# Kernel optimization log

Measured on AMD Instinct MI355X. Metric: run time of the kernel, lower is better.

The kernel has to match this reference:

```python
import jax, jax.numpy as jnp
import numpy as np

B_, S_, F_ = 4096, 512, 3
MAT_PTS = 128
N_OUT = 3
N_LAT = MAT_PTS * N_OUT  # 384
E, NU = 3130.0, 0.3
A_H, B_H, C_H = 64.8, 33.6, 0.003407
MU = E / (2.0 * (1.0 + NU))
LAM = E * NU / ((1.0 + NU) * (1.0 - 2.0 * NU))
NEWTON_ITERS = 12
VEC1 = jnp.array([1.0, 1.0, 1.0, 0.0], dtype=jnp.float32)  # identity in Voigt-4 (xx,yy,zz,xy)


def setup_inputs() -> dict:
    key = jax.random.key(0)
    k1, k2, k3 = jax.random.split(key, 3)
    x = jax.random.normal(k1, (B_, S_, F_), dtype=jnp.float32) * 0.01
    W1 = jax.random.normal(k2, (N_LAT, F_), dtype=jnp.float32) * (1.0 / np.sqrt(F_))
    W2 = jax.random.normal(k3, (N_OUT, N_LAT), dtype=jnp.float32) * (1.0 / np.sqrt(N_LAT))
    return {"x": x, "W1": W1, "W2": W2}


def _j2_update(state, eps):
    """J2 plane-strain return mapping with exponential hardening.
    state: (ep [N,4] tensorial plastic strain, kappa [N] eq. plastic strain)
    eps:   [N,3] engineering strain (exx, eyy, gxy).
    Returns new state and stress [N,3] (sxx, syy, sxy)."""
    ep, kappa = state
    e = jnp.stack([eps[:, 0], eps[:, 1], jnp.zeros_like(eps[:, 0]), 0.5 * eps[:, 2]], axis=-1)
    ee = e - ep                                   # elastic strain, tensorial
    tr = ee[:, 0] + ee[:, 1] + ee[:, 2]
    sig = 2.0 * MU * ee + LAM * tr[:, None] * VEC1  # trial stress (xx,yy,zz,xy)
    p = (sig[:, 0] + sig[:, 1] + sig[:, 2]) / 3.0
    s = sig - p[:, None] * VEC1                    # deviatoric
    q = jnp.sqrt(1.5 * (s[:, 0] ** 2 + s[:, 1] ** 2 + s[:, 2] ** 2 + 2.0 * s[:, 3] ** 2))
    sy = A_H - B_H * jnp.exp(-kappa / C_H)
    f = q - sy                                     # yield function (trial)

    def newton_step(dg, _):
        kp = kappa + dg
        r = q - 3.0 * MU * dg - (A_H - B_H * jnp.exp(-kp / C_H))
        dr = -3.0 * MU - (B_H / C_H) * jnp.exp(-kp / C_H)
        dg_new = jnp.maximum(dg - r / dr, 0.0)
        return dg_new, None

    dg0 = jnp.zeros_like(q)
    dg, _ = jax.lax.scan(newton_step, dg0, None, length=NEWTON_ITERS)
    dg = jnp.where(f > 0.0, dg, 0.0)
    q_safe = jnp.maximum(q, 1e-12)
    n = 1.5 * s / q_safe[:, None]                  # flow direction
    sig_new = sig - 2.0 * MU * dg[:, None] * n
    ep_new = ep + dg[:, None] * n
    kappa_new = kappa + dg
    stress = jnp.stack([sig_new[:, 0], sig_new[:, 1], sig_new[:, 3]], axis=-1)
    return (ep_new, kappa_new), stress


def _forward(x, W1, W2):
    B, S, F = x.shape
    N = B * MAT_PTS  # material points across the batch
    # fc1 is time-independent: apply to all timesteps at once
    h = jnp.einsum('bsf,lf->bsl', x, W1)                 # [B,S,n_latents]
    eps_seq = h.reshape(B, S, MAT_PTS, F_).transpose(1, 0, 2, 3).reshape(S, N, F_)
    ep0 = jnp.zeros((N, 4), dtype=x.dtype)
    k0 = jnp.zeros((N,), dtype=x.dtype)
    _, stresses = jax.lax.scan(_j2_update, (ep0, k0), eps_seq)  # [S,N,3]
    lat = stresses.reshape(S, B, N_LAT).transpose(1, 0, 2)      # [B,S,n_latents]
    return jnp.einsum('bsl,ol->bso', lat, W2)                   # [B,S,n_outputs]


def reference(x, W1, W2):
    return _forward(x, W1, W2)
```

## Files before the change

kernel.cpp:

```cpp
#include <hip/hip_runtime.h>
#include <math.h>

#define S_LEN 512
#define CH 8
#define NSEG 128
#define TBL_L0 -22.0f
#define TBL_INVH 4.0f
#define TBL_H 0.25f

typedef float v2f __attribute__((ext_vector_type(2)));

__device__ __forceinline__ float fast_rcp(float x) { return __builtin_amdgcn_rcpf(x); }
__device__ __forceinline__ float fast_rsq(float x) { return __builtin_amdgcn_rsqf(x); }
__device__ __forceinline__ float exp2s(float x)    { return __builtin_amdgcn_exp2f(x); }
__device__ __forceinline__ v2f rsqv(v2f a)  { return (v2f){fast_rsq(a.x), fast_rsq(a.y)}; }
__device__ __forceinline__ v2f maxv(v2f a, v2f b) { return __builtin_elementwise_max(a, b); }

template <int CTRL>
__device__ __forceinline__ float dpp_add(float v) {
    int vi = __builtin_bit_cast(int, v);
    int t  = __builtin_amdgcn_update_dpp(vi, vi, CTRL, 0xF, 0xF, true);
    return v + __builtin_bit_cast(float, t);
}

__global__ __launch_bounds__(128, 4) void prnn_kernel(
    const float* __restrict__ x,
    const float* __restrict__ W1,
    const float* __restrict__ W2,
    float* __restrict__ out)
{
    const double MUd = 3130.0 / 2.6;
    const double Cd  = 0.003407;
    const double K2d = 1.4426950408889634 / Cd;
    const float MU      = (float)MUd;
    const float THREE_MU= (float)(3.0 * MUd);
    const float C43     = (float)(4.0 * MUd / 3.0);
    const float C23     = (float)(2.0 * MUd / 3.0);
    const float CP      = (float)(7825.0 / 3.0);
    const float Cf      = (float)Cd;
    const float R3M     = (float)(1.0 / (3.0 * MUd));
    const float AR3M    = (float)(64.8 / (3.0 * MUd));
    const float MQ      = (float)(-K2d / (3.0 * MUd));
    const float KA0     = (float)(1.4492898 + (64.8 / (3.0 * MUd)) * K2d);
    const float K2      = (float)K2d;
    const float LOG2E   = 1.4426950408889634f;
    const float LN08    = (float)(0.8 * 0.6931471805599453);

    const int tid  = threadIdx.x;
    const int lane = tid & 63;
    const int wv   = tid >> 6;
    const int b    = blockIdx.x * 2 + wv;

    __shared__ float2 xs01[2][S_LEN];
    __shared__ float  xs2g[2][S_LEN];
    __shared__ float  part[2][CH][3][17];
    __shared__ float2 wtab[NSEG];

    {
        float wn = 0.0f;
        if (tid <= NSEG) {
            const float s = TBL_L0 + (float)tid * TBL_H;
            const float z = exp2s(s);
            float w = fmaxf(LN08 * s, z * (1.0f - z));
            #pragma unroll
            for (int it = 0; it < 4; ++it) {
                const float y   = exp2s(w * LOG2E);
                const float g   = w * y;
                const float F   = g - z;
                const float Fp  = g + y;
                const float den = Fp*Fp - 0.5f*((F*y)*(2.0f + w));
                w = w - (F*Fp)*fast_rcp(den);
            }
            wn = w;
            ((float*)wtab)[tid] = wn;
        }
        __syncthreads();
        float wnext = 0.0f;
        if (tid < NSEG) wnext = ((float*)wtab)[tid + 1];
        __syncthreads();
        if (tid < NSEG) {
            const float sl = (wnext - wn) * (Cf * TBL_INVH);
            const float bi = Cf * wn - sl * (TBL_L0 + (float)tid * TBL_H);
            wtab[tid] = (float2){sl, bi};
        }
        __syncthreads();
    }

    v2f D0[3], D1[3], D3[3], pv[3];
    #pragma unroll
    for (int f = 0; f < 3; ++f) {
        const int mA = lane, mB = lane + 64;
        v2f av = (v2f){ W1[(mA*3 + 0)*3 + f], W1[(mB*3 + 0)*3 + f] };
        v2f bv = (v2f){ W1[(mA*3 + 1)*3 + f], W1[(mB*3 + 1)*3 + f] };
        v2f cv = (v2f){ W1[(mA*3 + 2)*3 + f], W1[(mB*3 + 2)*3 + f] };
        D0[f] = C43*av - C23*bv;
        D1[f] = C43*bv - C23*av;
        D3[f] = MU*cv;
        pv[f] = CP*(av + bv);
    }
    v2f w2[3][3];
    #pragma unroll
    for (int o = 0; o < 3; ++o)
        #pragma unroll
        for (int j = 0; j < 3; ++j)
            w2[o][j] = (v2f){ W2[o*384 + lane*3 + j], W2[o*384 + (lane+64)*3 + j] };

    float gsel0, gsel1, gsel2;
    {
        v2f w2s[3];
        #pragma unroll
        for (int o = 0; o < 3; ++o) w2s[o] = w2[o][0] + w2[o][1];
        float G[3][3];
        #pragma unroll
        for (int o = 0; o < 3; ++o)
            #pragma unroll
            for (int f = 0; f < 3; ++f) {
                v2f gv = w2s[o] * pv[f];
                float g = gv.x + gv.y;
                #pragma unroll
                for (int m = 1; m < 64; m <<= 1) g += __shfl_xor(g, m, 64);
                G[o][f] = g;
            }
        const int ro = lane % 3;
        gsel0 = (ro == 0) ? G[0][0] : (ro == 1) ? G[1][0] : G[2][0];
        gsel1 = (ro == 0) ? G[0][1] : (ro == 1) ? G[1][1] : G[2][1];
        gsel2 = (ro == 0) ? G[0][2] : (ro == 1) ? G[1][2] : G[2][2];
    }

    const float* xb = x + (size_t)b * (S_LEN*3);
    for (int i = lane; i < S_LEN; i += 64) {
        xs01[wv][i] = (float2){ xb[i*3 + 0], xb[i*3 + 1] };
        xs2g[wv][i] = xb[i*3 + 2];
    }

    v2f sd0 = (v2f){0.f,0.f}, sd1 = sd0, sd3 = sd0;
    v2f ka2 = (v2f){KA0, KA0};
    float xp0 = 0.f, xp1 = 0.f, xp2 = 0.f;
    float* outb = out + (size_t)b * (S_LEN*3);

    #pragma unroll 1
    for (int tc = 0; tc < S_LEN; tc += CH) {
        #pragma unroll
        for (int tt = 0; tt < CH; ++tt) {
            const int t = tc + tt;
            const float2 x01 = xs01[wv][t];
            const float  xv2 = xs2g[wv][t];
            const float dx0 = x01.x - xp0, dx1 = x01.y - xp1, dx2 = xv2 - xp2;
            xp0 = x01.x; xp1 = x01.y; xp2 = xv2;

            v2f d0 = D0[0]*dx0 + D0[1]*dx1 + D0[2]*dx2 + sd0;
            v2f d1 = D1[0]*dx0 + D1[1]*dx1 + D1[2]*dx2 + sd1;
            v2f d3 = D3[0]*dx0 + D3[1]*dx1 + D3[2]*dx2 + sd3;

            v2f h   = d0*d0 + d1*d1 + d0*d1 + d3*d3;
            v2f dot = maxv(3.0f*h, (v2f){1e-24f,1e-24f});
            v2f qi  = rsqv(dot);
            v2f q   = dot * qi;

            v2f u0  = q*R3M - AR3M;
            v2f l2z = q*MQ + ka2;

            const float fix = __builtin_fmaf(l2z.x, TBL_INVH, -TBL_L0*TBL_INVH);
            const float fiy = __builtin_fmaf(l2z.y, TBL_INVH, -TBL_L0*TBL_INVH);
            int ix = (int)fix; ix = ix < 0 ? 0 : (ix > NSEG-1 ? NSEG-1 : ix);
            int iy = (int)fiy; iy = iy < 0 ? 0 : (iy > NSEG-1 ? NSEG-1 : iy);
            const float2 tx = wtab[ix];
            const float2 ty = wtab[iy];
            v2f cw = (v2f){ __builtin_fmaf(tx.x, l2z.x, tx.y),
                            __builtin_fmaf(ty.x, l2z.y, ty.y) };
            v2f dg = maxv(u0 + cw, (v2f){0.f,0.f});

            v2f n3q = -THREE_MU*qi;
            v2f u   = dg*n3q + 1.0f;
            sd0 = u*d0; sd1 = u*d1; sd3 = u*d3;
            ka2 = ka2 - K2*dg;

            v2f a0 = w2[0][0]*sd0 + w2[0][1]*sd1 + w2[0][2]*sd3;
            v2f a1 = w2[1][0]*sd0 + w2[1][1]*sd1 + w2[1][2]*sd3;
            v2f a2 = w2[2][0]*sd0 + w2[2][1]*sd1 + w2[2][2]*sd3;
            float c0 = a0.x + a0.y;
            float c1 = a1.x + a1.y;
            float c2 = a2.x + a2.y;

            c0 = dpp_add<0xB1>(c0); c0 = dpp_add<0x4E>(c0);
            c1 = dpp_add<0xB1>(c1); c1 = dpp_add<0x4E>(c1);
            c2 = dpp_add<0xB1>(c2); c2 = dpp_add<0x4E>(c2);
            if ((lane & 3) == 0) {
                const int g16 = lane >> 2;
                part[wv][tt][0][g16] = c0;
                part[wv][tt][1][g16] = c1;
                part[wv][tt][2][g16] = c2;
            }
        }
        if (lane < 24) {
            const int rtt = lane / 3;
            float s = 0.0f;
            #pragma unroll
            for (int g16 = 0; g16 < 16; ++g16) s += part[wv][rtt][lane - rtt*3][g16];
            const float2 xf01 = xs01[wv][tc + rtt];
            const float  xf2  = xs2g[wv][tc + rtt];
            s = __builtin_fmaf(gsel0, xf01.x, s);
            s = __builtin_fmaf(gsel1, xf01.y, s);
            s = __builtin_fmaf(gsel2, xf2,    s);
            outb[tc*3 + lane] = s;
        }
    }
}

extern "C" void kernel_launch(void* const* d_in, const int* in_sizes, int n_in,
                              void* d_out, int out_size, void* d_ws, size_t ws_size,
                              hipStream_t stream) {
    const float* x  = (const float*)d_in[0];
    const float* W1 = (const float*)d_in[1];
    const float* W2 = (const float*)d_in[2];
    float* out = (float*)d_out;
    prnn_kernel<<<2048, 128, 0, stream>>>(x, W1, W2, out);
}
```

Measured before the change: 307.0 us.

## Read x via wave-uniform scalar loads instead of LDS staging, drop v2f packing

Removes the LDS staging of each sequence's x and instead makes the batch index wave-uniform with readfirstlane, so x values can be fetched with scalar loads directly from global memory. The packed v2f arithmetic is replaced by scalar per-point FMA chains, and the table index upper clamp is dropped. This is meant to cut LDS traffic and instruction count in the serial time loop. In exchange, each step now does global and scalar-cache loads on the critical path, and dropping the clamp risks out-of-range table reads.

```diff
diff --git a/kernel.cpp b/kernel.cpp
--- a/kernel.cpp
+++ b/kernel.cpp
@@ -8,13 +8,9 @@
 #define TBL_INVH 4.0f
 #define TBL_H 0.25f
 
-typedef float v2f __attribute__((ext_vector_type(2)));
-
 __device__ __forceinline__ float fast_rcp(float x) { return __builtin_amdgcn_rcpf(x); }
 __device__ __forceinline__ float fast_rsq(float x) { return __builtin_amdgcn_rsqf(x); }
 __device__ __forceinline__ float exp2s(float x)    { return __builtin_amdgcn_exp2f(x); }
-__device__ __forceinline__ v2f rsqv(v2f a)  { return (v2f){fast_rsq(a.x), fast_rsq(a.y)}; }
-__device__ __forceinline__ v2f maxv(v2f a, v2f b) { return __builtin_elementwise_max(a, b); }
 
 template <int CTRL>
 __device__ __forceinline__ float dpp_add(float v) {
@@ -49,10 +45,8 @@
     const int tid  = threadIdx.x;
     const int lane = tid & 63;
     const int wv   = tid >> 6;
-    const int b    = blockIdx.x * 2 + wv;
-
-    __shared__ float2 xs01[2][S_LEN];
-    __shared__ float  xs2g[2][S_LEN];
+    const int bs   = __builtin_amdgcn_readfirstlane(blockIdx.x * 2 + wv);
+
     __shared__ float  part[2][CH][3][17];
     __shared__ float2 wtab[NSEG];
 
@@ -86,37 +80,38 @@
         __syncthreads();
     }
 
-    v2f D0[3], D1[3], D3[3], pv[3];
+    float D0[2][3], D1[2][3], D3[2][3], pvv[2][3], w2[2][3][3];
     #pragma unroll
-    for (int f = 0; f < 3; ++f) {
-        const int mA = lane, mB = lane + 64;
-        v2f av = (v2f){ W1[(mA*3 + 0)*3 + f], W1[(mB*3 + 0)*3 + f] };
-        v2f bv = (v2f){ W1[(mA*3 + 1)*3 + f], W1[(mB*3 + 1)*3 + f] };
-        v2f cv = (v2f){ W1[(mA*3 + 2)*3 + f], W1[(mB*3 + 2)*3 + f] };
-        D0[f] = C43*av - C23*bv;
-        D1[f] = C43*bv - C23*av;
-        D3[f] = MU*cv;
-        pv[f] = CP*(av + bv);
-    }
-    v2f w2[3][3];
-    #pragma unroll
-    for (int o = 0; o < 3; ++o)
-        #pragma unroll
-        for (int j = 0; j < 3; ++j)
-            w2[o][j] = (v2f){ W2[o*384 + lane*3 + j], W2[o*384 + (lane+64)*3 + j] };
+    for (int p = 0; p < 2; ++p) {
+        const int m = lane + 64*p;
+        #pragma unroll
+        for (int f = 0; f < 3; ++f) {
+            const float av = W1[(m*3 + 0)*3 + f];
+            const float bv = W1[(m*3 + 1)*3 + f];
+            const float cv = W1[(m*3 + 2)*3 + f];
+            D0[p][f]  = C43*av - C23*bv;
+            D1[p][f]  = C43*bv - C23*av;
+            D3[p][f]  = MU*cv;
+            pvv[p][f] = CP*(av + bv);
+        }
+        #pragma unroll
+        for (int o = 0; o < 3; ++o)
+            #pragma unroll
+            for (int j = 0; j < 3; ++j)
+                w2[p][o][j] = W2[o*384 + m*3 + j];
+    }
 
     float gsel0, gsel1, gsel2;
     {
-        v2f w2s[3];
-        #pragma unroll
-        for (int o = 0; o < 3; ++o) w2s[o] = w2[o][0] + w2[o][1];
         float G[3][3];
         #pragma unroll
         for (int o = 0; o < 3; ++o)
             #pragma unroll
             for (int f = 0; f < 3; ++f) {
-                v2f gv = w2s[o] * pv[f];
-                float g = gv.x + gv.y;
+                float g = 0.0f;
+                #pragma unroll
+                for (int p = 0; p < 2; ++p)
+                    g += (w2[p][o][0] + w2[p][o][1]) * pvv[p][f];
                 #pragma unroll
                 for (int m = 1; m < 64; m <<= 1) g += __shfl_xor(g, m, 64);
                 G[o][f] = g;
@@ -127,60 +122,71 @@
         gsel2 = (ro == 0) ? G[0][2] : (ro == 1) ? G[1][2] : G[2][2];
     }
 
-    const float* xb = x + (size_t)b * (S_LEN*3);
-    for (int i = lane; i < S_LEN; i += 64) {
-        xs01[wv][i] = (float2){ xb[i*3 + 0], xb[i*3 + 1] };
-        xs2g[wv][i] = xb[i*3 + 2];
-    }
-
-    v2f sd0 = (v2f){0.f,0.f}, sd1 = sd0, sd3 = sd0;
-    v2f ka2 = (v2f){KA0, KA0};
+    const float* xbs  = x   + (size_t)bs * (S_LEN*3);
+    float*       outb = out + (size_t)bs * (S_LEN*3);
+
+    float sd0[2] = {0.f,0.f}, sd1[2] = {0.f,0.f}, sd3[2] = {0.f,0.f};
+    float ka2[2] = {KA0, KA0};
     float xp0 = 0.f, xp1 = 0.f, xp2 = 0.f;
-    float* outb = out + (size_t)b * (S_LEN*3);
+
+    const int rtt0 = (lane < 24) ? (lane / 3) : 0;
 
     #pragma unroll 1
     for (int tc = 0; tc < S_LEN; tc += CH) {
+        const float* xrow = xbs + (tc + rtt0)*3;
+        const float fx0 = xrow[0], fx1 = xrow[1], fx2 = xrow[2];
+
         #pragma unroll
         for (int tt = 0; tt < CH; ++tt) {
             const int t = tc + tt;
-            const float2 x01 = xs01[wv][t];
-            const float  xv2 = xs2g[wv][t];
-            const float dx0 = x01.x - xp0, dx1 = x01.y - xp1, dx2 = xv2 - xp2;
-            xp0 = x01.x; xp1 = x01.y; xp2 = xv2;
-
-            v2f d0 = D0[0]*dx0 + D0[1]*dx1 + D0[2]*dx2 + sd0;
-            v2f d1 = D1[0]*dx0 + D1[1]*dx1 + D1[2]*dx2 + sd1;
-            v2f d3 = D3[0]*dx0 + D3[1]*dx1 + D3[2]*dx2 + sd3;
-
-            v2f h   = d0*d0 + d1*d1 + d0*d1 + d3*d3;
-            v2f dot = maxv(3.0f*h, (v2f){1e-24f,1e-24f});
-            v2f qi  = rsqv(dot);
-            v2f q   = dot * qi;
-
-            v2f u0  = q*R3M - AR3M;
-            v2f l2z = q*MQ + ka2;
-
-            const float fix = __builtin_fmaf(l2z.x, TBL_INVH, -TBL_L0*TBL_INVH);
-            const float fiy = __builtin_fmaf(l2z.y, TBL_INVH, -TBL_L0*TBL_INVH);
-            int ix = (int)fix; ix = ix < 0 ? 0 : (ix > NSEG-1 ? NSEG-1 : ix);
-            int iy = (int)fiy; iy = iy < 0 ? 0 : (iy > NSEG-1 ? NSEG-1 : iy);
-            const float2 tx = wtab[ix];
-            const float2 ty = wtab[iy];
-            v2f cw = (v2f){ __builtin_fmaf(tx.x, l2z.x, tx.y),
-                            __builtin_fmaf(ty.x, l2z.y, ty.y) };
-            v2f dg = maxv(u0 + cw, (v2f){0.f,0.f});
-
-            v2f n3q = -THREE_MU*qi;
-            v2f u   = dg*n3q + 1.0f;
-            sd0 = u*d0; sd1 = u*d1; sd3 = u*d3;
-            ka2 = ka2 - K2*dg;
-
-            v2f a0 = w2[0][0]*sd0 + w2[0][1]*sd1 + w2[0][2]*sd3;
-            v2f a1 = w2[1][0]*sd0 + w2[1][1]*sd1 + w2[1][2]*sd3;
-            v2f a2 = w2[2][0]*sd0 + w2[2][1]*sd1 + w2[2][2]*sd3;
-            float c0 = a0.x + a0.y;
-            float c1 = a1.x + a1.y;
-            float c2 = a2.x + a2.y;
+            const float x0 = xbs[t*3 + 0];
+            const float x1 = xbs[t*3 + 1];
+            const float x2 = xbs[t*3 + 2];
+            const float dx0 = x0 - xp0, dx1 = x1 - xp1, dx2 = x2 - xp2;
+            xp0 = x0; xp1 = x1; xp2 = x2;
+
+            float cc[2][3];
+            #pragma unroll
+            for (int p = 0; p < 2; ++p) {
+                const float d0 = __builtin_fmaf(D0[p][0], dx0,
+                                  __builtin_fmaf(D0[p][1], dx1,
+                                  __builtin_fmaf(D0[p][2], dx2, sd0[p])));
+                const float d1 = __builtin_fmaf(D1[p][0], dx0,
+                                  __builtin_fmaf(D1[p][1], dx1,
+                                  __builtin_fmaf(D1[p][2], dx2, sd1[p])));
+                const float d3 = __builtin_fmaf(D3[p][0], dx0,
+                                  __builtin_fmaf(D3[p][1], dx1,
+                                  __builtin_fmaf(D3[p][2], dx2, sd3[p])));
+
+                const float h   = __builtin_fmaf(d0, d0,
+                                   __builtin_fmaf(d1, d1,
+                                   __builtin_fmaf(d0, d1, d3*d3)));
+                const float dot = fmaxf(3.0f*h, 1e-24f);
+                const float qi  = fast_rsq(dot);
+                const float q   = dot * qi;
+
+                const float u0  = __builtin_fmaf(q, R3M, -AR3M);
+                const float l2z = __builtin_fmaf(q, MQ, ka2[p]);
+                const float fi  = __builtin_fmaf(l2z, TBL_INVH, -TBL_L0*TBL_INVH);
+                int ii = (int)fi; ii = ii < 0 ? 0 : ii;
+                const float2 tb = wtab[ii];
+                const float cw  = __builtin_fmaf(tb.x, l2z, tb.y);
+                const float dg  = fmaxf(u0 + cw, 0.0f);
+
+                const float n3q = -THREE_MU*qi;
+                const float u   = __builtin_fmaf(dg, n3q, 1.0f);
+                sd0[p] = u*d0; sd1[p] = u*d1; sd3[p] = u*d3;
+                ka2[p] = __builtin_fmaf(dg, -K2, ka2[p]);
+
+                #pragma unroll
+                for (int o = 0; o < 3; ++o)
+                    cc[p][o] = __builtin_fmaf(w2[p][o][0], sd0[p],
+                                __builtin_fmaf(w2[p][o][1], sd1[p],
+                                w2[p][o][2]*sd3[p]));
+            }
+            float c0 = cc[0][0] + cc[1][0];
+            float c1 = cc[0][1] + cc[1][1];
+            float c2 = cc[0][2] + cc[1][2];
 
             c0 = dpp_add<0xB1>(c0); c0 = dpp_add<0x4E>(c0);
             c1 = dpp_add<0xB1>(c1); c1 = dpp_add<0x4E>(c1);
@@ -197,11 +203,9 @@
             float s = 0.0f;
             #pragma unroll
             for (int g16 = 0; g16 < 16; ++g16) s += part[wv][rtt][lane - rtt*3][g16];
-            const float2 xf01 = xs01[wv][tc + rtt];
-            const float  xf2  = xs2g[wv][tc + rtt];
-            s = __builtin_fmaf(gsel0, xf01.x, s);
-            s = __builtin_fmaf(gsel1, xf01.y, s);
-            s = __builtin_fmaf(gsel2, xf2,    s);
+            s = __builtin_fmaf(gsel0, fx0, s);
+            s = __builtin_fmaf(gsel1, fx1, s);
+            s = __builtin_fmaf(gsel2, fx2, s);
             outb[tc*3 + lane] = s;
         }
     }
```

Result: slower. 327.2 us (+6.6%).
